# Performance work log

Measured on AMD Instinct MI355X. Metric: run time of the kernel, lower is better.

Reference implementation:

```python
import jax, jax.numpy as jnp
import numpy as np

N, F_IN, HID, HEADS, CLASSES, E = 50000, 256, 64, 4, 64, 800000
NEG_SLOPE = 0.2


def _glorot(key, shape):
    fan = shape[0] + shape[-1]
    return jax.random.normal(key, shape, jnp.float32) * jnp.sqrt(2.0 / fan)


def setup_inputs() -> dict:
    key = jax.random.key(0)
    ks = jax.random.split(key, 12)
    x = jax.random.normal(ks[0], (N, F_IN), jnp.float32)
    edge_index = jax.random.randint(ks[1], (2, E), 0, N, jnp.int32)
    d = {"x": x, "edge_index": edge_index}
    dims = [(F_IN, HID), (HEADS * HID, HID), (HEADS * HID, CLASSES)]
    k = 2
    for li, (din, dout) in enumerate(dims, start=1):
        d[f"W{li}"] = _glorot(ks[k], (din, HEADS * dout)); k += 1
        d[f"a_src{li}"] = _glorot(ks[k], (HEADS, dout)); k += 1
        d[f"a_dst{li}"] = _glorot(ks[k], (HEADS, dout)); k += 1
        bdim = HEADS * dout if li < 3 else dout
        d[f"b{li}"] = jnp.zeros((bdim,), jnp.float32)
    return d


def _gat_layer(x, src, dst, W, a_src, a_dst, b, out_dim, concat):
    n = x.shape[0]
    h = (x @ W).reshape(n, HEADS, out_dim)            # [N,H,D]
    al_s = jnp.einsum("nhd,hd->nh", h, a_src)         # [N,H]
    al_d = jnp.einsum("nhd,hd->nh", h, a_dst)
    logits = jax.nn.leaky_relu(al_s[src] + al_d[dst], NEG_SLOPE)  # [E,H]
    # segment softmax over destination nodes (self-loops guarantee non-empty)
    m = jax.ops.segment_max(logits, dst, num_segments=n)
    e = jnp.exp(logits - m[dst])
    denom = jax.ops.segment_sum(e, dst, num_segments=n)
    att = e / denom[dst]                              # [E,H]
    msg = h[src] * att[:, :, None]                    # [E,H,D]
    out = jax.ops.segment_sum(msg, dst, num_segments=n)
    out = out.reshape(n, HEADS * out_dim) if concat else out.mean(axis=1)
    return out + b


def reference(x, edge_index, W1, a_src1, a_dst1, b1, W2, a_src2, a_dst2, b2,
              W3, a_src3, a_dst3, b3):
    loop = jnp.arange(N, dtype=edge_index.dtype)
    src = jnp.concatenate([edge_index[0], loop])
    dst = jnp.concatenate([edge_index[1], loop])
    h = _gat_layer(x, src, dst, W1, a_src1, a_dst1, b1, HID, True)
    h = jax.nn.elu(h)  # dropout is identity in eval mode
    h = _gat_layer(h, src, dst, W2, a_src2, a_dst2, b2, HID, True)
    h = jax.nn.elu(h)
    h = _gat_layer(h, src, dst, W3, a_src3, a_dst3, b3, CLASSES, False)
    return jax.nn.log_softmax(h, axis=-1)
```

## Files before the change

kernel.cpp:

```cpp
#include <hip/hip_runtime.h>
#include <stdint.h>

typedef __bf16 bf16x8 __attribute__((ext_vector_type(8)));
typedef float f32x4 __attribute__((ext_vector_type(4)));
typedef unsigned short u16x8 __attribute__((ext_vector_type(8)));

__device__ __forceinline__ unsigned short f2bf(float f){
  union { float f; unsigned u; } c; c.f = f;
  unsigned u = c.u;
  unsigned r = u + 0x7FFFu + ((u >> 16) & 1u);
  return (unsigned short)(r >> 16);
}

__global__ void k_hist(const int* __restrict__ ei, int E, int Nn, int* __restrict__ counts){
  int total = E + Nn;
  for (int e = blockIdx.x*blockDim.x + threadIdx.x; e < total; e += gridDim.x*blockDim.x){
    int d = (e < E) ? ei[E + e] : (e - E);
    atomicAdd(&counts[d], 1);
  }
}

__global__ __launch_bounds__(1024) void k_scan1(const int* __restrict__ counts, int* __restrict__ rowptr,
                                                int* __restrict__ bsum, int n){
  __shared__ int wsum[17];
  int tid = threadIdx.x, lane = tid & 63, wid = tid >> 6;
  int i = blockIdx.x*1024 + tid;
  int v = (i < n) ? counts[i] : 0;
  int iv = v;
  #pragma unroll
  for (int off = 1; off < 64; off <<= 1){
    int t = __shfl_up(iv, off, 64);
    if (lane >= off) iv += t;
  }
  if (lane == 63) wsum[wid] = iv;
  __syncthreads();
  if (tid == 0){
    int run = 0;
    for (int w = 0; w < 16; ++w){ int t = wsum[w]; wsum[w] = run; run += t; }
    wsum[16] = run;
  }
  __syncthreads();
  if (i < n) rowptr[i + 1] = iv + wsum[wid];
  if (tid == 0) bsum[blockIdx.x] = wsum[16];
}

__global__ __launch_bounds__(1024) void k_scan2(int* __restrict__ bsum, int nb){
  __shared__ int wsum[17];
  int tid = threadIdx.x, lane = tid & 63, wid = tid >> 6;
  int v = (tid < nb) ? bsum[tid] : 0;
  int iv = v;
  #pragma unroll
  for (int off = 1; off < 64; off <<= 1){
    int t = __shfl_up(iv, off, 64);
    if (lane >= off) iv += t;
  }
  if (lane == 63) wsum[wid] = iv;
  __syncthreads();
  if (tid == 0){
    int run = 0;
    for (int w = 0; w < 16; ++w){ int t = wsum[w]; wsum[w] = run; run += t; }
  }
  __syncthreads();
  if (tid < nb) bsum[tid] = iv + wsum[wid] - v;
}

__global__ void k_scan3(int* __restrict__ rowptr, const int* __restrict__ bsum, int n){
  int i = blockIdx.x*blockDim.x + threadIdx.x;
  if (i == 0) rowptr[0] = 0;
  if (i < n) rowptr[i + 1] += bsum[i >> 10];
}

__global__ void k_scatter(const int* __restrict__ ei, int E, int Nn, const int* __restrict__ rowptr,
                          int* __restrict__ cursor, int* __restrict__ srcs){
  int total = E + Nn;
  for (int e = blockIdx.x*blockDim.x + threadIdx.x; e < total; e += gridDim.x*blockDim.x){
    int s, d;
    if (e < E){ s = ei[e]; d = ei[E + e]; } else { s = d = e - E; }
    int pos = rowptr[d] + atomicAdd(&cursor[d], 1);
    srcs[pos] = s;
  }
}

__global__ void k_transpose_w(const float* __restrict__ W, unsigned short* __restrict__ Wt){
  int t = blockIdx.x*blockDim.x + threadIdx.x;
  int k = t >> 8, c = t & 255;
  Wt[c*256 + k] = f2bf(W[k*256 + c]);
}

template<bool AF32>
__global__ __launch_bounds__(512) void k_gemm2(const void* __restrict__ Av,
                                               const unsigned short* __restrict__ Wt,
                                               const float* __restrict__ asrc,
                                               const float* __restrict__ adst,
                                               unsigned short* __restrict__ H,
                                               float* __restrict__ als,
                                               float* __restrict__ ald,
                                               int Nn){
  __shared__ unsigned short As[64][264];
  int tid = threadIdx.x;
  int wid = tid >> 6, lane = tid & 63;
  int w = wid & 3, rh = wid >> 2;
  int row0 = blockIdx.x * 64;

  const unsigned short* a16 = (const unsigned short*)Av;
  const float*          a32 = (const float*)Av;

  #pragma unroll
  for (int it = 0; it < 4; ++it){
    int li = it*512 + tid;
    int rr = li >> 5, c16 = li & 31;
    int gr = row0 + rr; if (gr >= Nn) gr = Nn - 1;
    if (AF32){
      const float* ap = a32 + (size_t)gr*256 + c16*8;
      float4 v0 = *reinterpret_cast<const float4*>(ap);
      float4 v1 = *reinterpret_cast<const float4*>(ap + 4);
      union { uint4 q; unsigned short s[8]; } u;
      u.s[0]=f2bf(v0.x); u.s[1]=f2bf(v0.y); u.s[2]=f2bf(v0.z); u.s[3]=f2bf(v0.w);
      u.s[4]=f2bf(v1.x); u.s[5]=f2bf(v1.y); u.s[6]=f2bf(v1.z); u.s[7]=f2bf(v1.w);
      *reinterpret_cast<uint4*>(&As[rr][c16*8]) = u.q;
    } else {
      uint4 v = *reinterpret_cast<const uint4*>(a16 + (size_t)gr*256 + c16*8);
      *reinterpret_cast<uint4*>(&As[rr][c16*8]) = v;
    }
  }
  __syncthreads();

  int r = lane & 15, kg = lane >> 4;
  f32x4 acc[2][4] = {};

  #pragma unroll
  for (int k0 = 0; k0 < 256; k0 += 32){
    bf16x8 a0 = *reinterpret_cast<const bf16x8*>(&As[rh*32 +      r][kg*8 + k0]);
    bf16x8 a1 = *reinterpret_cast<const bf16x8*>(&As[rh*32 + 16 + r][kg*8 + k0]);
    #pragma unroll
    for (int c = 0; c < 4; ++c){
      bf16x8 bfr = *reinterpret_cast<const bf16x8*>(Wt + (size_t)(w*64 + c*16 + r)*256 + kg*8 + k0);
      acc[0][c] = __builtin_amdgcn_mfma_f32_16x16x32_bf16(a0, bfr, acc[0][c], 0, 0, 0);
      acc[1][c] = __builtin_amdgcn_mfma_f32_16x16x32_bf16(a1, bfr, acc[1][c], 0, 0, 0);
    }
  }

  int rbase = row0 + rh*32;
  #pragma unroll
  for (int n = 0; n < 2; ++n){
    #pragma unroll
    for (int i = 0; i < 4; ++i){
      int row = rbase + n*16 + kg*4 + i;
      if (row < Nn){
        #pragma unroll
        for (int c = 0; c < 4; ++c)
          H[(size_t)row*256 + w*64 + c*16 + r] = f2bf(acc[n][c][i]);
      }
    }
  }

  float as_c[4], ad_c[4];
  #pragma unroll
  for (int c = 0; c < 4; ++c){
    as_c[c] = asrc[w*64 + c*16 + r];
    ad_c[c] = adst[w*64 + c*16 + r];
  }
  #pragma unroll
  for (int n = 0; n < 2; ++n){
    #pragma unroll
    for (int i = 0; i < 4; ++i){
      float ps = acc[n][0][i]*as_c[0] + acc[n][1][i]*as_c[1]
               + acc[n][2][i]*as_c[2] + acc[n][3][i]*as_c[3];
      float pd = acc[n][0][i]*ad_c[0] + acc[n][1][i]*ad_c[1]
               + acc[n][2][i]*ad_c[2] + acc[n][3][i]*ad_c[3];
      #pragma unroll
      for (int off = 1; off < 16; off <<= 1){
        ps += __shfl_xor(ps, off, 64);
        pd += __shfl_xor(pd, off, 64);
      }
      int row = rbase + n*16 + kg*4 + i;
      if (r == 0 && row < Nn){
        als[row*4 + w] = ps;
        ald[row*4 + w] = pd;
      }
    }
  }
}

template<int MODE>
__global__ void k_gather3(const unsigned short* __restrict__ Hm, const int* __restrict__ rowptr,
                          const int* __restrict__ srcs, const float* __restrict__ als,
                          const float* __restrict__ ald, const float* __restrict__ bias,
                          unsigned short* __restrict__ actout, float* __restrict__ finalout, int Nn){
  int gid = blockIdx.x*blockDim.x + threadIdx.x;
  int node = gid >> 6, lane = gid & 63;
  if (node >= Nn) return;
  int half = lane >> 5;
  int l32  = lane & 31;
  int fbase = l32 * 8;
  int hd = l32 >> 3;
  unsigned voff_feat = (unsigned)(l32 * 16);

  int beg = rowptr[node], deg = rowptr[node + 1] - beg;
  float4 adv = *reinterpret_cast<const float4*>(ald + (size_t)node*4);
  float aldh = (hd == 0) ? adv.x : (hd == 1) ? adv.y : (hd == 2) ? adv.z : adv.w;

  float acc[4][8];
  #pragma unroll
  for (int u = 0; u < 4; ++u)
    #pragma unroll
    for (int i = 0; i < 8; ++i) acc[u][i] = 0.f;
  float sw = 0.f;

  const char* Hb = (const char*)Hm;
  const char* Ab = (const char*)als;

  for (int cb = 0; cb < deg; cb += 64){
    int chunk = min(64, deg - cb);
    int mysrc = (cb + lane < deg) ? srcs[beg + cb + lane] : 0;
    int jmax8 = chunk & ~7;
    int j = 0;
    for (; j < jmax8; j += 8){
      #pragma unroll
      for (int u = 0; u < 4; ++u){
        int e0 = j + 2*u;
        int sA = __builtin_amdgcn_readlane(mysrc, e0);
        int sB = __builtin_amdgcn_readlane(mysrc, e0 + 1);
        int sM = half ? sB : sA;
        uint4 hw = *reinterpret_cast<const uint4*>(Hb + (unsigned)sM*512u + voff_feat);
        float av = *reinterpret_cast<const float*>(Ab + ((unsigned)sM << 4) + ((unsigned)hd << 2));
        float l = av + aldh; l = l > 0.f ? l : 0.2f*l;
        float wgt = __expf(l);
        sw += wgt;
        float h0 = __uint_as_float(hw.x << 16);
        float h1 = __uint_as_float(hw.x & 0xffff0000u);
        float h2 = __uint_as_float(hw.y << 16);
        float h3 = __uint_as_float(hw.y & 0xffff0000u);
        float h4 = __uint_as_float(hw.z << 16);
        float h5 = __uint_as_float(hw.z & 0xffff0000u);
        float h6 = __uint_as_float(hw.w << 16);
        float h7 = __uint_as_float(hw.w & 0xffff0000u);
        acc[u][0] = fmaf(wgt, h0, acc[u][0]);
        acc[u][1] = fmaf(wgt, h1, acc[u][1]);
        acc[u][2] = fmaf(wgt, h2, acc[u][2]);
        acc[u][3] = fmaf(wgt, h3, acc[u][3]);
        acc[u][4] = fmaf(wgt, h4, acc[u][4]);
        acc[u][5] = fmaf(wgt, h5, acc[u][5]);
        acc[u][6] = fmaf(wgt, h6, acc[u][6]);
        acc[u][7] = fmaf(wgt, h7, acc[u][7]);
      }
    }
    for (; j < chunk; j += 2){
      int eA = j;
      int eB = (j + 1 < chunk) ? (j + 1) : j;
      int sA = __builtin_amdgcn_readlane(mysrc, eA);
      int sB = __builtin_amdgcn_readlane(mysrc, eB);
      int sM = half ? sB : sA;
      uint4 hw = *reinterpret_cast<const uint4*>(Hb + (unsigned)sM*512u + voff_feat);
      float av = *reinterpret_cast<const float*>(Ab + ((unsigned)sM << 4) + ((unsigned)hd << 2));
      float l = av + aldh; l = l > 0.f ? l : 0.2f*l;
      float wgt = __expf(l);
      if (j + half >= chunk) wgt = 0.f;
      sw += wgt;
      float h0 = __uint_as_float(hw.x << 16);
      float h1 = __uint_as_float(hw.x & 0xffff0000u);
      float h2 = __uint_as_float(hw.y << 16);
      float h3 = __uint_as_float(hw.y & 0xffff0000u);
      float h4 = __uint_as_float(hw.z << 16);
      float h5 = __uint_as_float(hw.z & 0xffff0000u);
      float h6 = __uint_as_float(hw.w << 16);
      float h7 = __uint_as_float(hw.w & 0xffff0000u);
      acc[0][0] = fmaf(wgt, h0, acc[0][0]);
      acc[0][1] = fmaf(wgt, h1, acc[0][1]);
      acc[0][2] = fmaf(wgt, h2, acc[0][2]);
      acc[0][3] = fmaf(wgt, h3, acc[0][3]);
      acc[0][4] = fmaf(wgt, h4, acc[0][4]);
      acc[0][5] = fmaf(wgt, h5, acc[0][5]);
      acc[0][6] = fmaf(wgt, h6, acc[0][6]);
      acc[0][7] = fmaf(wgt, h7, acc[0][7]);
    }
  }

  float accf[8];
  #pragma unroll
  for (int i = 0; i < 8; ++i){
    float t = acc[0][i] + acc[1][i] + acc[2][i] + acc[3][i];
    t += __shfl_xor(t, 32, 64);
    accf[i] = t;
  }
  float s = sw + __shfl_xor(sw, 32, 64);
  float inv = 1.f / s;

  if (MODE == 0){
    if (lane < 32){
      float4 b0 = *reinterpret_cast<const float4*>(bias + fbase);
      float4 b1 = *reinterpret_cast<const float4*>(bias + fbase + 4);
      float o[8];
      o[0] = accf[0]*inv + b0.x; o[1] = accf[1]*inv + b0.y;
      o[2] = accf[2]*inv + b0.z; o[3] = accf[3]*inv + b0.w;
      o[4] = accf[4]*inv + b1.x; o[5] = accf[5]*inv + b1.y;
      o[6] = accf[6]*inv + b1.z; o[7] = accf[7]*inv + b1.w;
      u16x8 pk;
      #pragma unroll
      for (int i = 0; i < 8; ++i){
        float v = o[i];
        v = v > 0.f ? v : __expf(v) - 1.f;
        pk[i] = f2bf(v);
      }
      *reinterpret_cast<u16x8*>(actout + (size_t)node*256 + fbase) = pk;
    }
  } else {
    float v[8];
    #pragma unroll
    for (int i = 0; i < 8; ++i){
      float t = accf[i]*inv;
      t += __shfl_xor(t, 8, 64);
      t += __shfl_xor(t, 16, 64);
      v[i] = t;
    }
    int k = l32 & 7;
    float4 b0 = *reinterpret_cast<const float4*>(bias + k*8);
    float4 b1 = *reinterpret_cast<const float4*>(bias + k*8 + 4);
    v[0] = v[0]*0.25f + b0.x; v[1] = v[1]*0.25f + b0.y;
    v[2] = v[2]*0.25f + b0.z; v[3] = v[3]*0.25f + b0.w;
    v[4] = v[4]*0.25f + b1.x; v[5] = v[5]*0.25f + b1.y;
    v[6] = v[6]*0.25f + b1.z; v[7] = v[7]*0.25f + b1.w;
    float mx = v[0];
    #pragma unroll
    for (int i = 1; i < 8; ++i) mx = fmaxf(mx, v[i]);
    #pragma unroll
    for (int off = 1; off < 8; off <<= 1) mx = fmaxf(mx, __shfl_xor(mx, off, 64));
    float se = 0.f;
    #pragma unroll
    for (int i = 0; i < 8; ++i) se += __expf(v[i] - mx);
    #pragma unroll
    for (int off = 1; off < 8; off <<= 1) se += __shfl_xor(se, off, 64);
    float lse = mx + __logf(se);
    if (lane < 8){
      float4 o0, o1;
      o0.x = v[0]-lse; o0.y = v[1]-lse; o0.z = v[2]-lse; o0.w = v[3]-lse;
      o1.x = v[4]-lse; o1.y = v[5]-lse; o1.z = v[6]-lse; o1.w = v[7]-lse;
      float* dst = finalout + (size_t)node*64 + lane*8;
      *reinterpret_cast<float4*>(dst)     = o0;
      *reinterpret_cast<float4*>(dst + 4) = o1;
    }
  }
}

extern "C" void kernel_launch(void* const* d_in, const int* in_sizes, int n_in,
                              void* d_out, int out_size, void* d_ws, size_t ws_size,
                              hipStream_t stream){
  const float* x     = (const float*)d_in[0];
  const int*   ei    = (const int*)  d_in[1];
  const float* W1    = (const float*)d_in[2];
  const float* asrc1 = (const float*)d_in[3];
  const float* adst1 = (const float*)d_in[4];
  const float* b1    = (const float*)d_in[5];
  const float* W2    = (const float*)d_in[6];
  const float* asrc2 = (const float*)d_in[7];
  const float* adst2 = (const float*)d_in[8];
  const float* b2    = (const float*)d_in[9];
  const float* W3    = (const float*)d_in[10];
  const float* asrc3 = (const float*)d_in[11];
  const float* adst3 = (const float*)d_in[12];
  const float* b3    = (const float*)d_in[13];
  float* out = (float*)d_out;

  int N = in_sizes[0] / 256;
  int E = in_sizes[1] / 2;

  char* p = (char*)d_ws;
  auto carve = [&](size_t bytes){ void* r = (void*)p; p += (bytes + 511) & ~(size_t)511; return r; };
  unsigned short* bufA = (unsigned short*)carve((size_t)N*256*2);
  unsigned short* bufH = (unsigned short*)carve((size_t)N*256*2);
  unsigned short* bufB = (unsigned short*)carve((size_t)N*256*2);
  unsigned short* wt1  = (unsigned short*)carve(256*256*2);
  unsigned short* wt2  = (unsigned short*)carve(256*256*2);
  unsigned short* wt3  = (unsigned short*)carve(256*256*2);
  float* als   = (float*)carve((size_t)N*4*4);
  float* ald   = (float*)carve((size_t)N*4*4);
  int* rowptr  = (int*)carve((size_t)(N+1)*4);
  int* cursor  = (int*)carve((size_t)N*4);
  int* bsum    = (int*)carve((size_t)1024*4);
  int* srcs    = (int*)carve((size_t)(E+N)*4);

  hipMemsetAsync(cursor, 0, (size_t)N*4, stream);
  k_hist<<<2048, 256, 0, stream>>>(ei, E, N, cursor);
  int nb = (N + 1023) / 1024;
  k_scan1<<<nb, 1024, 0, stream>>>(cursor, rowptr, bsum, N);
  k_scan2<<<1, 1024, 0, stream>>>(bsum, nb);
  k_scan3<<<(N + 255)/256, 256, 0, stream>>>(rowptr, bsum, N);
  hipMemsetAsync(cursor, 0, (size_t)N*4, stream);
  k_scatter<<<2048, 256, 0, stream>>>(ei, E, N, rowptr, cursor, srcs);

  k_transpose_w<<<256, 256, 0, stream>>>(W1, wt1);
  k_transpose_w<<<256, 256, 0, stream>>>(W2, wt2);
  k_transpose_w<<<256, 256, 0, stream>>>(W3, wt3);

  int gemm_grid  = (N + 63) / 64;
  int nodeblocks = (N*64 + 255)/256;

  k_gemm2<true><<<gemm_grid, 512, 0, stream>>>(x, wt1, asrc1, adst1, bufH, als, ald, N);
  k_gather3<0><<<nodeblocks, 256, 0, stream>>>(bufH, rowptr, srcs, als, ald, b1, bufB, nullptr, N);
  k_gemm2<false><<<gemm_grid, 512, 0, stream>>>(bufB, wt2, asrc2, adst2, bufH, als, ald, N);
  k_gather3<0><<<nodeblocks, 256, 0, stream>>>(bufH, rowptr, srcs, als, ald, b2, bufA, nullptr, N);
  k_gemm2<false><<<gemm_grid, 512, 0, stream>>>(bufA, wt3, asrc3, adst3, bufH, als, ald, N);
  k_gather3<1><<<nodeblocks, 256, 0, stream>>>(bufH, rowptr, srcs, als, ald, b3, nullptr, out, N);
}
```

Baseline: 425.4 us.

## Persistent double-buffered GEMM, per-chunk attention weights in LDS, fused CSR setup

The GEMM becomes a persistent kernel. Each block handles two row tiles and prefetches the next tile into registers while the current tile runs through MFMA. The gather kernel now computes attention weights once per edge per chunk: it does a vectorized als load and writes the weights to LDS. Previously every lane recomputed exp per edge per head. Setup also fuses the cursor init into the scan, which drops one memset and the rowptr read in scatter, and merges the three weight transposes into one launch. The risks are halved GEMM grid occupancy and an LDS read/write hazard between chunks in the gather, since the only guard is a waitcnt and no barrier.

Measured after the change: 418.0 us. Within noise of the previous version (-1.7%).

```diff
diff --git a/kernel.cpp b/kernel.cpp
--- a/kernel.cpp
+++ b/kernel.cpp
@@ -64,95 +64,91 @@
   if (tid < nb) bsum[tid] = iv + wsum[wid] - v;
 }
 
-__global__ void k_scan3(int* __restrict__ rowptr, const int* __restrict__ bsum, int n){
+__global__ void k_scan3(int* __restrict__ rowptr, const int* __restrict__ bsum,
+                        const int* __restrict__ counts, int* __restrict__ cursor, int n){
   int i = blockIdx.x*blockDim.x + threadIdx.x;
   if (i == 0) rowptr[0] = 0;
-  if (i < n) rowptr[i + 1] += bsum[i >> 10];
-}
-
-__global__ void k_scatter(const int* __restrict__ ei, int E, int Nn, const int* __restrict__ rowptr,
+  if (i < n){
+    int v = rowptr[i + 1] + bsum[i >> 10];
+    rowptr[i + 1] = v;
+    cursor[i] = v - counts[i];
+  }
+}
+
+__global__ void k_scatter(const int* __restrict__ ei, int E, int Nn,
                           int* __restrict__ cursor, int* __restrict__ srcs){
   int total = E + Nn;
   for (int e = blockIdx.x*blockDim.x + threadIdx.x; e < total; e += gridDim.x*blockDim.x){
     int s, d;
     if (e < E){ s = ei[e]; d = ei[E + e]; } else { s = d = e - E; }
-    int pos = rowptr[d] + atomicAdd(&cursor[d], 1);
+    int pos = atomicAdd(&cursor[d], 1);
     srcs[pos] = s;
   }
 }
 
-__global__ void k_transpose_w(const float* __restrict__ W, unsigned short* __restrict__ Wt){
+__global__ void k_transpose_all(const float* __restrict__ W1, const float* __restrict__ W2,
+                                const float* __restrict__ W3, unsigned short* __restrict__ wt1,
+                                unsigned short* __restrict__ wt2, unsigned short* __restrict__ wt3){
   int t = blockIdx.x*blockDim.x + threadIdx.x;
-  int k = t >> 8, c = t & 255;
+  int which = t >> 16, li = t & 65535;
+  int k = li >> 8, c = li & 255;
+  const float* W = (which == 0) ? W1 : (which == 1) ? W2 : W3;
+  unsigned short* Wt = (which == 0) ? wt1 : (which == 1) ? wt2 : wt3;
   Wt[c*256 + k] = f2bf(W[k*256 + c]);
 }
 
 template<bool AF32>
-__global__ __launch_bounds__(512) void k_gemm2(const void* __restrict__ Av,
+__global__ __launch_bounds__(512) void k_gemm3(const void* __restrict__ Av,
                                                const unsigned short* __restrict__ Wt,
                                                const float* __restrict__ asrc,
                                                const float* __restrict__ adst,
                                                unsigned short* __restrict__ H,
                                                float* __restrict__ als,
                                                float* __restrict__ ald,
-                                               int Nn){
+                                               int Nn, int T, int G){
   __shared__ unsigned short As[64][264];
   int tid = threadIdx.x;
   int wid = tid >> 6, lane = tid & 63;
   int w = wid & 3, rh = wid >> 2;
-  int row0 = blockIdx.x * 64;
+  int r = lane & 15, kg = lane >> 4;
 
   const unsigned short* a16 = (const unsigned short*)Av;
   const float*          a32 = (const float*)Av;
 
-  #pragma unroll
-  for (int it = 0; it < 4; ++it){
-    int li = it*512 + tid;
-    int rr = li >> 5, c16 = li & 31;
-    int gr = row0 + rr; if (gr >= Nn) gr = Nn - 1;
-    if (AF32){
-      const float* ap = a32 + (size_t)gr*256 + c16*8;
-      float4 v0 = *reinterpret_cast<const float4*>(ap);
-      float4 v1 = *reinterpret_cast<const float4*>(ap + 4);
-      union { uint4 q; unsigned short s[8]; } u;
-      u.s[0]=f2bf(v0.x); u.s[1]=f2bf(v0.y); u.s[2]=f2bf(v0.z); u.s[3]=f2bf(v0.w);
-      u.s[4]=f2bf(v1.x); u.s[5]=f2bf(v1.y); u.s[6]=f2bf(v1.z); u.s[7]=f2bf(v1.w);
-      *reinterpret_cast<uint4*>(&As[rr][c16*8]) = u.q;
-    } else {
-      uint4 v = *reinterpret_cast<const uint4*>(a16 + (size_t)gr*256 + c16*8);
-      *reinterpret_cast<uint4*>(&As[rr][c16*8]) = v;
-    }
-  }
-  __syncthreads();
-
-  int r = lane & 15, kg = lane >> 4;
-  f32x4 acc[2][4] = {};
-
-  #pragma unroll
-  for (int k0 = 0; k0 < 256; k0 += 32){
-    bf16x8 a0 = *reinterpret_cast<const bf16x8*>(&As[rh*32 +      r][kg*8 + k0]);
-    bf16x8 a1 = *reinterpret_cast<const bf16x8*>(&As[rh*32 + 16 + r][kg*8 + k0]);
-    #pragma unroll
-    for (int c = 0; c < 4; ++c){
-      bf16x8 bfr = *reinterpret_cast<const bf16x8*>(Wt + (size_t)(w*64 + c*16 + r)*256 + kg*8 + k0);
-      acc[0][c] = __builtin_amdgcn_mfma_f32_16x16x32_bf16(a0, bfr, acc[0][c], 0, 0, 0);
-      acc[1][c] = __builtin_amdgcn_mfma_f32_16x16x32_bf16(a1, bfr, acc[1][c], 0, 0, 0);
-    }
-  }
-
-  int rbase = row0 + rh*32;
-  #pragma unroll
-  for (int n = 0; n < 2; ++n){
-    #pragma unroll
-    for (int i = 0; i < 4; ++i){
-      int row = rbase + n*16 + kg*4 + i;
-      if (row < Nn){
-        #pragma unroll
-        for (int c = 0; c < 4; ++c)
-          H[(size_t)row*256 + w*64 + c*16 + r] = f2bf(acc[n][c][i]);
-      }
-    }
-  }
+  uint4  sreg[4];
+  float4 sregf[4][2];
+
+  auto load_tile = [&](int t){
+    #pragma unroll
+    for (int it = 0; it < 4; ++it){
+      int li = it*512 + tid;
+      int rr = li >> 5, c16 = li & 31;
+      int gr = t*64 + rr; if (gr >= Nn) gr = Nn - 1;
+      if (AF32){
+        const float* ap = a32 + (size_t)gr*256 + c16*8;
+        sregf[it][0] = *reinterpret_cast<const float4*>(ap);
+        sregf[it][1] = *reinterpret_cast<const float4*>(ap + 4);
+      } else {
+        sreg[it] = *reinterpret_cast<const uint4*>(a16 + (size_t)gr*256 + c16*8);
+      }
+    }
+  };
+  auto write_lds = [&](){
+    #pragma unroll
+    for (int it = 0; it < 4; ++it){
+      int li = it*512 + tid;
+      int rr = li >> 5, c16 = li & 31;
+      if (AF32){
+        float4 v0 = sregf[it][0], v1 = sregf[it][1];
+        union { uint4 q; unsigned short s[8]; } u;
+        u.s[0]=f2bf(v0.x); u.s[1]=f2bf(v0.y); u.s[2]=f2bf(v0.z); u.s[3]=f2bf(v0.w);
+        u.s[4]=f2bf(v1.x); u.s[5]=f2bf(v1.y); u.s[6]=f2bf(v1.z); u.s[7]=f2bf(v1.w);
+        *reinterpret_cast<uint4*>(&As[rr][c16*8]) = u.q;
+      } else {
+        *reinterpret_cast<uint4*>(&As[rr][c16*8]) = sreg[it];
+      }
+    }
+  };
 
   float as_c[4], ad_c[4];
   #pragma unroll
@@ -160,73 +156,128 @@
     as_c[c] = asrc[w*64 + c*16 + r];
     ad_c[c] = adst[w*64 + c*16 + r];
   }
-  #pragma unroll
-  for (int n = 0; n < 2; ++n){
-    #pragma unroll
-    for (int i = 0; i < 4; ++i){
-      float ps = acc[n][0][i]*as_c[0] + acc[n][1][i]*as_c[1]
-               + acc[n][2][i]*as_c[2] + acc[n][3][i]*as_c[3];
-      float pd = acc[n][0][i]*ad_c[0] + acc[n][1][i]*ad_c[1]
-               + acc[n][2][i]*ad_c[2] + acc[n][3][i]*ad_c[3];
+
+  int t = blockIdx.x;
+  if (t >= T) return;
+  load_tile(t);
+
+  for (;;){
+    write_lds();
+    __syncthreads();
+    int tn = t + G;
+    bool more = (tn < T);
+    if (more) load_tile(tn);
+
+    f32x4 acc[2][4] = {};
+    #pragma unroll
+    for (int k0 = 0; k0 < 256; k0 += 32){
+      bf16x8 a0 = *reinterpret_cast<const bf16x8*>(&As[rh*32 +      r][kg*8 + k0]);
+      bf16x8 a1 = *reinterpret_cast<const bf16x8*>(&As[rh*32 + 16 + r][kg*8 + k0]);
       #pragma unroll
-      for (int off = 1; off < 16; off <<= 1){
-        ps += __shfl_xor(ps, off, 64);
-        pd += __shfl_xor(pd, off, 64);
-      }
-      int row = rbase + n*16 + kg*4 + i;
-      if (r == 0 && row < Nn){
-        als[row*4 + w] = ps;
-        ald[row*4 + w] = pd;
-      }
-    }
+      for (int c = 0; c < 4; ++c){
+        bf16x8 bfr = *reinterpret_cast<const bf16x8*>(Wt + (size_t)(w*64 + c*16 + r)*256 + kg*8 + k0);
+        acc[0][c] = __builtin_amdgcn_mfma_f32_16x16x32_bf16(a0, bfr, acc[0][c], 0, 0, 0);
+        acc[1][c] = __builtin_amdgcn_mfma_f32_16x16x32_bf16(a1, bfr, acc[1][c], 0, 0, 0);
+      }
+    }
+
+    int rbase = t*64 + rh*32;
+    #pragma unroll
+    for (int n = 0; n < 2; ++n){
+      #pragma unroll
+      for (int i = 0; i < 4; ++i){
+        int row = rbase + n*16 + kg*4 + i;
+        if (row < Nn){
+          #pragma unroll
+          for (int c = 0; c < 4; ++c)
+            H[(size_t)row*256 + w*64 + c*16 + r] = f2bf(acc[n][c][i]);
+        }
+      }
+    }
+    #pragma unroll
+    for (int n = 0; n < 2; ++n){
+      #pragma unroll
+      for (int i = 0; i < 4; ++i){
+        float ps = acc[n][0][i]*as_c[0] + acc[n][1][i]*as_c[1]
+                 + acc[n][2][i]*as_c[2] + acc[n][3][i]*as_c[3];
+        float pd = acc[n][0][i]*ad_c[0] + acc[n][1][i]*ad_c[1]
+                 + acc[n][2][i]*ad_c[2] + acc[n][3][i]*ad_c[3];
+        #pragma unroll
+        for (int off = 1; off < 16; off <<= 1){
+          ps += __shfl_xor(ps, off, 64);
+          pd += __shfl_xor(pd, off, 64);
+        }
+        int row = rbase + n*16 + kg*4 + i;
+        if (r == 0 && row < Nn){
+          als[row*4 + w] = ps;
+          ald[row*4 + w] = pd;
+        }
+      }
+    }
+
+    if (!more) break;
+    __syncthreads();
+    t = tn;
   }
 }
 
 template<int MODE>
-__global__ void k_gather3(const unsigned short* __restrict__ Hm, const int* __restrict__ rowptr,
-                          const int* __restrict__ srcs, const float* __restrict__ als,
-                          const float* __restrict__ ald, const float* __restrict__ bias,
+__global__ __launch_bounds__(256) void k_gather4(const unsigned short* __restrict__ Hm,
+                          const int* __restrict__ rowptr, const int* __restrict__ srcs,
+                          const float* __restrict__ als, const float* __restrict__ ald,
+                          const float* __restrict__ bias,
                           unsigned short* __restrict__ actout, float* __restrict__ finalout, int Nn){
+  __shared__ float wlds[4][64][4];
   int gid = blockIdx.x*blockDim.x + threadIdx.x;
   int node = gid >> 6, lane = gid & 63;
   if (node >= Nn) return;
+  int wv_id = threadIdx.x >> 6;
   int half = lane >> 5;
   int l32  = lane & 31;
   int fbase = l32 * 8;
   int hd = l32 >> 3;
-  unsigned voff_feat = (unsigned)(l32 * 16);
+  unsigned voff = (unsigned)(l32 * 16);
 
   int beg = rowptr[node], deg = rowptr[node + 1] - beg;
   float4 adv = *reinterpret_cast<const float4*>(ald + (size_t)node*4);
-  float aldh = (hd == 0) ? adv.x : (hd == 1) ? adv.y : (hd == 2) ? adv.z : adv.w;
 
   float acc[4][8];
   #pragma unroll
   for (int u = 0; u < 4; ++u)
     #pragma unroll
     for (int i = 0; i < 8; ++i) acc[u][i] = 0.f;
-  float sw = 0.f;
+  float sw0 = 0.f, sw1 = 0.f, sw2 = 0.f, sw3 = 0.f;
 
   const char* Hb = (const char*)Hm;
-  const char* Ab = (const char*)als;
+  const float* wrow = &wlds[wv_id][0][0];
 
   for (int cb = 0; cb < deg; cb += 64){
     int chunk = min(64, deg - cb);
-    int mysrc = (cb + lane < deg) ? srcs[beg + cb + lane] : 0;
-    int jmax8 = chunk & ~7;
-    int j = 0;
-    for (; j < jmax8; j += 8){
+    bool valid = (lane < chunk);
+    int mysrc = valid ? srcs[beg + cb + lane] : 0;
+
+    float4 a = *reinterpret_cast<const float4*>(als + (size_t)mysrc*4);
+    float l0 = a.x + adv.x; l0 = l0 > 0.f ? l0 : 0.2f*l0;
+    float l1 = a.y + adv.y; l1 = l1 > 0.f ? l1 : 0.2f*l1;
+    float l2 = a.z + adv.z; l2 = l2 > 0.f ? l2 : 0.2f*l2;
+    float l3 = a.w + adv.w; l3 = l3 > 0.f ? l3 : 0.2f*l3;
+    float4 wvv;
+    wvv.x = valid ? __expf(l0) : 0.f;
+    wvv.y = valid ? __expf(l1) : 0.f;
+    wvv.z = valid ? __expf(l2) : 0.f;
+    wvv.w = valid ? __expf(l3) : 0.f;
+    sw0 += wvv.x; sw1 += wvv.y; sw2 += wvv.z; sw3 += wvv.w;
+    *reinterpret_cast<float4*>(&wlds[wv_id][lane][0]) = wvv;
+    asm volatile("s_waitcnt lgkmcnt(0)" ::: "memory");
+    __builtin_amdgcn_sched_barrier(0);
+
+    for (int e = 0; e < chunk; e += 8){
       #pragma unroll
       for (int u = 0; u < 4; ++u){
-        int e0 = j + 2*u;
-        int sA = __builtin_amdgcn_readlane(mysrc, e0);
-        int sB = __builtin_amdgcn_readlane(mysrc, e0 + 1);
-        int sM = half ? sB : sA;
-        uint4 hw = *reinterpret_cast<const uint4*>(Hb + (unsigned)sM*512u + voff_feat);
-        float av = *reinterpret_cast<const float*>(Ab + ((unsigned)sM << 4) + ((unsigned)hd << 2));
-        float l = av + aldh; l = l > 0.f ? l : 0.2f*l;
-        float wgt = __expf(l);
-        sw += wgt;
+        int pe = e + 2*u;
+        int sM = __shfl(mysrc, pe + half, 64);
+        uint4 hw = *reinterpret_cast<const uint4*>(Hb + (unsigned)sM*512u + voff);
+        float wgt = wrow[(unsigned)(pe + half)*4u + (unsigned)hd];
         float h0 = __uint_as_float(hw.x << 16);
         float h1 = __uint_as_float(hw.x & 0xffff0000u);
         float h2 = __uint_as_float(hw.y << 16);
@@ -245,36 +296,17 @@
         acc[u][7] = fmaf(wgt, h7, acc[u][7]);
       }
     }
-    for (; j < chunk; j += 2){
-      int eA = j;
-      int eB = (j + 1 < chunk) ? (j + 1) : j;
-      int sA = __builtin_amdgcn_readlane(mysrc, eA);
-      int sB = __builtin_amdgcn_readlane(mysrc, eB);
-      int sM = half ? sB : sA;
-      uint4 hw = *reinterpret_cast<const uint4*>(Hb + (unsigned)sM*512u + voff_feat);
-      float av = *reinterpret_cast<const float*>(Ab + ((unsigned)sM << 4) + ((unsigned)hd << 2));
-      float l = av + aldh; l = l > 0.f ? l : 0.2f*l;
-      float wgt = __expf(l);
-      if (j + half >= chunk) wgt = 0.f;
-      sw += wgt;
-      float h0 = __uint_as_float(hw.x << 16);
-      float h1 = __uint_as_float(hw.x & 0xffff0000u);
-      float h2 = __uint_as_float(hw.y << 16);
-      float h3 = __uint_as_float(hw.y & 0xffff0000u);
-      float h4 = __uint_as_float(hw.z << 16);
-      float h5 = __uint_as_float(hw.z & 0xffff0000u);
-      float h6 = __uint_as_float(hw.w << 16);
-      float h7 = __uint_as_float(hw.w & 0xffff0000u);
-      acc[0][0] = fmaf(wgt, h0, acc[0][0]);
-      acc[0][1] = fmaf(wgt, h1, acc[0][1]);
-      acc[0][2] = fmaf(wgt, h2, acc[0][2]);
-      acc[0][3] = fmaf(wgt, h3, acc[0][3]);
-      acc[0][4] = fmaf(wgt, h4, acc[0][4]);
-      acc[0][5] = fmaf(wgt, h5, acc[0][5]);
-      acc[0][6] = fmaf(wgt, h6, acc[0][6]);
-      acc[0][7] = fmaf(wgt, h7, acc[0][7]);
-    }
-  }
+  }
+
+  #pragma unroll
+  for (int off = 1; off < 64; off <<= 1){
+    sw0 += __shfl_xor(sw0, off, 64);
+    sw1 += __shfl_xor(sw1, off, 64);
+    sw2 += __shfl_xor(sw2, off, 64);
+    sw3 += __shfl_xor(sw3, off, 64);
+  }
+  float sden = (hd == 0) ? sw0 : (hd == 1) ? sw1 : (hd == 2) ? sw2 : sw3;
+  float inv = 1.f / sden;
 
   float accf[8];
   #pragma unroll
@@ -283,8 +315,6 @@
     t += __shfl_xor(t, 32, 64);
     accf[i] = t;
   }
-  float s = sw + __shfl_xor(sw, 32, 64);
-  float inv = 1.f / s;
 
   if (MODE == 0){
     if (lane < 32){
@@ -372,33 +402,32 @@
   unsigned short* wt1  = (unsigned short*)carve(256*256*2);
   unsigned short* wt2  = (unsigned short*)carve(256*256*2);
   unsigned short* wt3  = (unsigned short*)carve(256*256*2);
-  float* als   = (float*)carve((size_t)N*4*4);
-  float* ald   = (float*)carve((size_t)N*4*4);
-  int* rowptr  = (int*)carve((size_t)(N+1)*4);
-  int* cursor  = (int*)carve((size_t)N*4);
-  int* bsum    = (int*)carve((size_t)1024*4);
-  int* srcs    = (int*)carve((size_t)(E+N)*4);
-
-  hipMemsetAsync(cursor, 0, (size_t)N*4, stream);
-  k_hist<<<2048, 256, 0, stream>>>(ei, E, N, cursor);
+  float* als    = (float*)carve((size_t)N*4*4);
+  float* ald    = (float*)carve((size_t)N*4*4);
+  int* rowptr   = (int*)carve((size_t)(N+1)*4);
+  int* counts   = (int*)carve((size_t)N*4);
+  int* cursor   = (int*)carve((size_t)N*4);
+  int* bsum     = (int*)carve((size_t)1024*4);
+  int* srcs     = (int*)carve((size_t)(E+N)*4);
+
+  hipMemsetAsync(counts, 0, (size_t)N*4, stream);
+  k_hist<<<2048, 256, 0, stream>>>(ei, E, N, counts);
   int nb = (N + 1023) / 1024;
-  k_scan1<<<nb, 1024, 0, stream>>>(cursor, rowptr, bsum, N);
+  k_scan1<<<nb, 1024, 0, stream>>>(counts, rowptr, bsum, N);
   k_scan2<<<1, 1024, 0, stream>>>(bsum, nb);
-  k_scan3<<<(N + 255)/256, 256, 0, stream>>>(rowptr, bsum, N);
-  hipMemsetAsync(cursor, 0, (size_t)N*4, stream);
-  k_scatter<<<2048, 256, 0, stream>>>(ei, E, N, rowptr, cursor, srcs);
-
-  k_transpose_w<<<256, 256, 0, stream>>>(W1, wt1);
-  k_transpose_w<<<256, 256, 0, stream>>>(W2, wt2);
-  k_transpose_w<<<256, 256, 0, stream>>>(W3, wt3);
-
-  int gemm_grid  = (N + 63) / 64;
+  k_scan3<<<(N + 255)/256, 256, 0, stream>>>(rowptr, bsum, counts, cursor, N);
+  k_scatter<<<2048, 256, 0, stream>>>(ei, E, N, cursor, srcs);
+
+  k_transpose_all<<<768, 256, 0, stream>>>(W1, W2, W3, wt1, wt2, wt3);
+
+  int T = (N + 63) / 64;
+  int G = (T + 1) / 2;
   int nodeblocks = (N*64 + 255)/256;
 
-  k_gemm2<true><<<gemm_grid, 512, 0, stream>>>(x, wt1, asrc1, adst1, bufH, als, ald, N);
-  k_gather3<0><<<nodeblocks, 256, 0, stream>>>(bufH, rowptr, srcs, als, ald, b1, bufB, nullptr, N);
-  k_gemm2<false><<<gemm_grid, 512, 0, stream>>>(bufB, wt2, asrc2, adst2, bufH, als, ald, N);
-  k_gather3<0><<<nodeblocks, 256, 0, stream>>>(bufH, rowptr, srcs, als, ald, b2, bufA, nullptr, N);
-  k_gemm2<false><<<gemm_grid, 512, 0, stream>>>(bufA, wt3, asrc3, adst3, bufH, als, ald, N);
-  k_gather3<1><<<nodeblocks, 256, 0, stream>>>(bufH, rowptr, srcs, als, ald, b3, nullptr, out, N);
-}
+  k_gemm3<true><<<G, 512, 0, stream>>>(x, wt1, asrc1, adst1, bufH, als, ald, N, T, G);
+  k_gather4<0><<<nodeblocks, 256, 0, stream>>>(bufH, rowptr, srcs, als, ald, b1, bufB, nullptr, N);
+  k_gemm3<false><<<G, 512, 0, stream>>>(bufB, wt2, asrc2, adst2, bufH, als, ald, N, T, G);
+  k_gather4<0><<<nodeblocks, 256, 0, stream>>>(bufH, rowptr, srcs, als, ald, b2, bufA, nullptr, N);
+  k_gemm3<false><<<G, 512, 0, stream>>>(bufA, wt3, asrc3, adst3, bufH, als, ald, N, T, G);
+  k_gather4<1><<<nodeblocks, 256, 0, stream>>>(bufH, rowptr, srcs, als, ald, b3, nullptr, out, N);
+}
```

## Fuse prep kernels, pre-convert x to bf16, shrink GEMM tiles, drop cursor memset

Applied to the files above, without the earlier changes.

Several changes land together. The scan now initialises the scatter cursor to the row start, which removes a memset and a rowptr read in the scatter. The three weight transposes and a new full conversion of x to bf16 are merged into one launch. The GEMM moves from 64-row, 512-thread blocks to 32-row, 256-thread blocks, which doubles the grid and halves the shared memory per block. The cost is an extra pass over x (read fp32, write bf16) in exchange for a simpler first-layer GEMM and fewer launches.

Result: no change. 432.3 us (+1.6%).

```diff
diff --git a/kernel.cpp b/kernel.cpp
--- a/kernel.cpp
+++ b/kernel.cpp
@@ -64,31 +64,52 @@
   if (tid < nb) bsum[tid] = iv + wsum[wid] - v;
 }
 
-__global__ void k_scan3(int* __restrict__ rowptr, const int* __restrict__ bsum, int n){
+__global__ void k_scan3(int* __restrict__ rowptr, const int* __restrict__ bsum,
+                        const int* __restrict__ counts, int* __restrict__ cursor, int n){
   int i = blockIdx.x*blockDim.x + threadIdx.x;
   if (i == 0) rowptr[0] = 0;
-  if (i < n) rowptr[i + 1] += bsum[i >> 10];
-}
-
-__global__ void k_scatter(const int* __restrict__ ei, int E, int Nn, const int* __restrict__ rowptr,
+  if (i < n){
+    int v = rowptr[i + 1] + bsum[i >> 10];
+    rowptr[i + 1] = v;
+    cursor[i] = v - counts[i];
+  }
+}
+
+__global__ void k_scatter(const int* __restrict__ ei, int E, int Nn,
                           int* __restrict__ cursor, int* __restrict__ srcs){
   int total = E + Nn;
   for (int e = blockIdx.x*blockDim.x + threadIdx.x; e < total; e += gridDim.x*blockDim.x){
     int s, d;
     if (e < E){ s = ei[e]; d = ei[E + e]; } else { s = d = e - E; }
-    int pos = rowptr[d] + atomicAdd(&cursor[d], 1);
+    int pos = atomicAdd(&cursor[d], 1);
     srcs[pos] = s;
   }
 }
 
-__global__ void k_transpose_w(const float* __restrict__ W, unsigned short* __restrict__ Wt){
-  int t = blockIdx.x*blockDim.x + threadIdx.x;
-  int k = t >> 8, c = t & 255;
-  Wt[c*256 + k] = f2bf(W[k*256 + c]);
-}
-
-template<bool AF32>
-__global__ __launch_bounds__(512) void k_gemm2(const void* __restrict__ Av,
+__global__ void k_prep(const float* __restrict__ x, unsigned short* __restrict__ xbf, int nx4, int nconv,
+                       const float* __restrict__ W1, const float* __restrict__ W2,
+                       const float* __restrict__ W3, unsigned short* __restrict__ wt1,
+                       unsigned short* __restrict__ wt2, unsigned short* __restrict__ wt3){
+  int b = blockIdx.x;
+  if (b < nconv){
+    int i = b*256 + threadIdx.x;
+    if (i < nx4){
+      float4 v = reinterpret_cast<const float4*>(x)[i];
+      ushort4 o;
+      o.x = f2bf(v.x); o.y = f2bf(v.y); o.z = f2bf(v.z); o.w = f2bf(v.w);
+      reinterpret_cast<ushort4*>(xbf)[i] = o;
+    }
+  } else {
+    int t = (b - nconv)*256 + threadIdx.x;
+    int which = t >> 16, li = t & 65535;
+    int k = li >> 8, c = li & 255;
+    const float* W = (which == 0) ? W1 : (which == 1) ? W2 : W3;
+    unsigned short* Wt = (which == 0) ? wt1 : (which == 1) ? wt2 : wt3;
+    Wt[c*256 + k] = f2bf(W[k*256 + c]);
+  }
+}
+
+__global__ __launch_bounds__(256) void k_gemm5(const unsigned short* __restrict__ A,
                                                const unsigned short* __restrict__ Wt,
                                                const float* __restrict__ asrc,
                                                const float* __restrict__ adst,
@@ -96,42 +117,27 @@
                                                float* __restrict__ als,
                                                float* __restrict__ ald,
                                                int Nn){
-  __shared__ unsigned short As[64][264];
+  __shared__ unsigned short As[32][264];
   int tid = threadIdx.x;
-  int wid = tid >> 6, lane = tid & 63;
-  int w = wid & 3, rh = wid >> 2;
-  int row0 = blockIdx.x * 64;
-
-  const unsigned short* a16 = (const unsigned short*)Av;
-  const float*          a32 = (const float*)Av;
+  int w = tid >> 6, lane = tid & 63;
+  int r = lane & 15, kg = lane >> 4;
+  int row0 = blockIdx.x * 32;
 
   #pragma unroll
   for (int it = 0; it < 4; ++it){
-    int li = it*512 + tid;
+    int li = it*256 + tid;
     int rr = li >> 5, c16 = li & 31;
     int gr = row0 + rr; if (gr >= Nn) gr = Nn - 1;
-    if (AF32){
-      const float* ap = a32 + (size_t)gr*256 + c16*8;
-      float4 v0 = *reinterpret_cast<const float4*>(ap);
-      float4 v1 = *reinterpret_cast<const float4*>(ap + 4);
-      union { uint4 q; unsigned short s[8]; } u;
-      u.s[0]=f2bf(v0.x); u.s[1]=f2bf(v0.y); u.s[2]=f2bf(v0.z); u.s[3]=f2bf(v0.w);
-      u.s[4]=f2bf(v1.x); u.s[5]=f2bf(v1.y); u.s[6]=f2bf(v1.z); u.s[7]=f2bf(v1.w);
-      *reinterpret_cast<uint4*>(&As[rr][c16*8]) = u.q;
-    } else {
-      uint4 v = *reinterpret_cast<const uint4*>(a16 + (size_t)gr*256 + c16*8);
-      *reinterpret_cast<uint4*>(&As[rr][c16*8]) = v;
-    }
+    uint4 v = *reinterpret_cast<const uint4*>(A + (size_t)gr*256 + c16*8);
+    *reinterpret_cast<uint4*>(&As[rr][c16*8]) = v;
   }
   __syncthreads();
 
-  int r = lane & 15, kg = lane >> 4;
   f32x4 acc[2][4] = {};
-
   #pragma unroll
   for (int k0 = 0; k0 < 256; k0 += 32){
-    bf16x8 a0 = *reinterpret_cast<const bf16x8*>(&As[rh*32 +      r][kg*8 + k0]);
-    bf16x8 a1 = *reinterpret_cast<const bf16x8*>(&As[rh*32 + 16 + r][kg*8 + k0]);
+    bf16x8 a0 = *reinterpret_cast<const bf16x8*>(&As[r][kg*8 + k0]);
+    bf16x8 a1 = *reinterpret_cast<const bf16x8*>(&As[16 + r][kg*8 + k0]);
     #pragma unroll
     for (int c = 0; c < 4; ++c){
       bf16x8 bfr = *reinterpret_cast<const bf16x8*>(Wt + (size_t)(w*64 + c*16 + r)*256 + kg*8 + k0);
@@ -140,12 +146,11 @@
     }
   }
 
-  int rbase = row0 + rh*32;
   #pragma unroll
   for (int n = 0; n < 2; ++n){
     #pragma unroll
     for (int i = 0; i < 4; ++i){
-      int row = rbase + n*16 + kg*4 + i;
+      int row = row0 + n*16 + kg*4 + i;
       if (row < Nn){
         #pragma unroll
         for (int c = 0; c < 4; ++c)
@@ -173,7 +178,7 @@
         ps += __shfl_xor(ps, off, 64);
         pd += __shfl_xor(pd, off, 64);
       }
-      int row = rbase + n*16 + kg*4 + i;
+      int row = row0 + n*16 + kg*4 + i;
       if (r == 0 && row < Nn){
         als[row*4 + w] = ps;
         ald[row*4 + w] = pd;
@@ -366,39 +371,39 @@
 
   char* p = (char*)d_ws;
   auto carve = [&](size_t bytes){ void* r = (void*)p; p += (bytes + 511) & ~(size_t)511; return r; };
-  unsigned short* bufA = (unsigned short*)carve((size_t)N*256*2);
+  unsigned short* xbf  = (unsigned short*)carve((size_t)N*256*2);
   unsigned short* bufH = (unsigned short*)carve((size_t)N*256*2);
   unsigned short* bufB = (unsigned short*)carve((size_t)N*256*2);
   unsigned short* wt1  = (unsigned short*)carve(256*256*2);
   unsigned short* wt2  = (unsigned short*)carve(256*256*2);
   unsigned short* wt3  = (unsigned short*)carve(256*256*2);
-  float* als   = (float*)carve((size_t)N*4*4);
-  float* ald   = (float*)carve((size_t)N*4*4);
-  int* rowptr  = (int*)carve((size_t)(N+1)*4);
-  int* cursor  = (int*)carve((size_t)N*4);
-  int* bsum    = (int*)carve((size_t)1024*4);
-  int* srcs    = (int*)carve((size_t)(E+N)*4);
-
-  hipMemsetAsync(cursor, 0, (size_t)N*4, stream);
-  k_hist<<<2048, 256, 0, stream>>>(ei, E, N, cursor);
+  float* als    = (float*)carve((size_t)N*4*4);
+  float* ald    = (float*)carve((size_t)N*4*4);
+  int* rowptr   = (int*)carve((size_t)(N+1)*4);
+  int* counts   = (int*)carve((size_t)N*4);
+  int* cursor   = (int*)carve((size_t)N*4);
+  int* bsum     = (int*)carve((size_t)1024*4);
+  int* srcs     = (int*)carve((size_t)(E+N)*4);
+
+  hipMemsetAsync(counts, 0, (size_t)N*4, stream);
+  k_hist<<<2048, 256, 0, stream>>>(ei, E, N, counts);
   int nb = (N + 1023) / 1024;
-  k_scan1<<<nb, 1024, 0, stream>>>(cursor, rowptr, bsum, N);
+  k_scan1<<<nb, 1024, 0, stream>>>(counts, rowptr, bsum, N);
   k_scan2<<<1, 1024, 0, stream>>>(bsum, nb);
-  k_scan3<<<(N + 255)/256, 256, 0, stream>>>(rowptr, bsum, N);
-  hipMemsetAsync(cursor, 0, (size_t)N*4, stream);
-  k_scatter<<<2048, 256, 0, stream>>>(ei, E, N, rowptr, cursor, srcs);
-
-  k_transpose_w<<<256, 256, 0, stream>>>(W1, wt1);
-  k_transpose_w<<<256, 256, 0, stream>>>(W2, wt2);
-  k_transpose_w<<<256, 256, 0, stream>>>(W3, wt3);
-
-  int gemm_grid  = (N + 63) / 64;
+  k_scan3<<<(N + 255)/256, 256, 0, stream>>>(rowptr, bsum, counts, cursor, N);
+  k_scatter<<<2048, 256, 0, stream>>>(ei, E, N, cursor, srcs);
+
+  int nx4 = (N*256)/4;
+  int nconv = (nx4 + 255)/256;
+  k_prep<<<nconv + 768, 256, 0, stream>>>(x, xbf, nx4, nconv, W1, W2, W3, wt1, wt2, wt3);
+
+  int gemm_grid  = (N + 31) / 32;
   int nodeblocks = (N*64 + 255)/256;
 
-  k_gemm2<true><<<gemm_grid, 512, 0, stream>>>(x, wt1, asrc1, adst1, bufH, als, ald, N);
+  k_gemm5<<<gemm_grid, 256, 0, stream>>>(xbf, wt1, asrc1, adst1, bufH, als, ald, N);
   k_gather3<0><<<nodeblocks, 256, 0, stream>>>(bufH, rowptr, srcs, als, ald, b1, bufB, nullptr, N);
-  k_gemm2<false><<<gemm_grid, 512, 0, stream>>>(bufB, wt2, asrc2, adst2, bufH, als, ald, N);
-  k_gather3<0><<<nodeblocks, 256, 0, stream>>>(bufH, rowptr, srcs, als, ald, b2, bufA, nullptr, N);
-  k_gemm2<false><<<gemm_grid, 512, 0, stream>>>(bufA, wt3, asrc3, adst3, bufH, als, ald, N);
+  k_gemm5<<<gemm_grid, 256, 0, stream>>>(bufB, wt2, asrc2, adst2, bufH, als, ald, N);
+  k_gather3<0><<<nodeblocks, 256, 0, stream>>>(bufH, rowptr, srcs, als, ald, b2, xbf, nullptr, N);
+  k_gemm5<<<gemm_grid, 256, 0, stream>>>(xbf, wt3, asrc3, adst3, bufH, als, ald, N);
   k_gather3<1><<<nodeblocks, 256, 0, stream>>>(bufH, rowptr, srcs, als, ald, b3, nullptr, out, N);
 }
```
